# Kernel optimization log

Hardware: AMD Instinct MI355X
Metric: run time of the kernel (lower is better)

## Reference

```python
import jax, jax.numpy as jnp
import numpy as np

N, T_IN, PRE_LEN = 4096, 8, 12
E, H = 64, 128
MAX_NEI_DIS = 5.0


def _lstm_cell(x, h, c, Wih, Whh, bih, bhh):
    # torch.nn.LSTMCell math; gate order i, f, g, o
    gates = x @ Wih.T + bih + h @ Whh.T + bhh
    i, f, g, o = jnp.split(gates, 4, axis=-1)
    i = jax.nn.sigmoid(i)
    f = jax.nn.sigmoid(f)
    g = jnp.tanh(g)
    o = jax.nn.sigmoid(o)
    c_new = f * c + i * g
    return o * jnp.tanh(c_new), c_new


def _social_pool(pos, hidden):
    # sum hidden[j] over j with ||pos_j - pos_i|| < MAX_NEI_DIS (self included)
    d2 = jnp.sum((pos[:, None, :] - pos[None, :, :]) ** 2, axis=-1)  # [N,N]
    mask = (d2 < MAX_NEI_DIS * MAX_NEI_DIS).astype(hidden.dtype)
    return mask @ hidden  # [N,H]


def setup_inputs() -> dict:
    key = jax.random.key(0)
    ks = jax.random.split(key, 10)
    tracks = jax.random.normal(ks[0], (N, T_IN, 2), dtype=jnp.float32) * 20.0
    s = 0.05
    return {
        "tracks": tracks,
        "We": jax.random.normal(ks[1], (E, 2), dtype=jnp.float32) * s,
        "be": jax.random.normal(ks[2], (E,), dtype=jnp.float32) * s,
        "Wih": jax.random.normal(ks[3], (4 * H, H + E), dtype=jnp.float32) * s,
        "Whh": jax.random.normal(ks[4], (4 * H, H), dtype=jnp.float32) * s,
        "bih": jax.random.normal(ks[5], (4 * H,), dtype=jnp.float32) * s,
        "bhh": jax.random.normal(ks[6], (4 * H,), dtype=jnp.float32) * s,
        "Wd": jax.random.normal(ks[7], (2, H), dtype=jnp.float32) * s,
        "bd": jax.random.normal(ks[8], (2,), dtype=jnp.float32) * s,
    }


def reference(tracks, We, be, Wih, Whh, bih, bhh, Wd, bd):
    n = tracks.shape[0]
    emb = lambda p: p @ We.T + be

    # ---- group_encode ----
    x0 = jnp.concatenate([emb(tracks[:, 0]), jnp.zeros((n, H), tracks.dtype)], axis=1)
    h, c = _lstm_cell(x0, jnp.zeros((n, H), tracks.dtype), jnp.zeros((n, H), tracks.dtype),
                      Wih, Whh, bih, bhh)

    def enc_step(carry, pos):
        h, c = carry
        sh = _social_pool(pos, h)
        x = jnp.concatenate([emb(pos), sh], axis=1)
        h, c = _lstm_cell(x, h, c, Wih, Whh, bih, bhh)
        return (h, c), None

    # frame_idx = 0 .. input_len-2 -> positions at frames 0..6
    enc_pos = jnp.swapaxes(tracks[:, : T_IN - 1], 0, 1)  # [7, N, 2]
    (h, c), _ = jax.lax.scan(enc_step, (h, c), enc_pos)

    # ---- decode ----
    def dec_step(carry, _):
        h, c, last = carry
        sh = _social_pool(last, h)
        x = jnp.concatenate([emb(last), sh], axis=1)
        h, c = _lstm_cell(x, h, c, Wih, Whh, bih, bhh)
        delta = h @ Wd.T + bd
        last = last + delta
        return (h, c, last), last[0]

    last = tracks[:, -1]
    _, preds0 = jax.lax.scan(dec_step, (h, c, last), None, length=PRE_LEN)
    # returned group_track[0]: original 8 frames + 12 predicted positions
    return jnp.concatenate([tracks[0], preds0], axis=0)  # [20, 2]
```

## Files before the change

### kernel.cpp

```cpp
#include <hip/hip_runtime.h>
#include <hip/hip_bf16.h>

#define N_AG   4096
#define T_IN   8
#define PRELEN 12
#define EDIM   64
#define HDIM   128
#define KTOT   320
#define GDIM   512
#define KI     10
#define LOSCALE 2048.0f

typedef _Float16 f16x8 __attribute__((ext_vector_type(8)));
typedef _Float16 f16x2 __attribute__((ext_vector_type(2)));
typedef float    f32x4 __attribute__((ext_vector_type(4)));


__global__ __launch_bounds__(256) void init_kernel(
    const float* __restrict__ tracks,
    const float* __restrict__ Wih, const float* __restrict__ Whh,
    const float* __restrict__ bih, const float* __restrict__ bhh,
    float* __restrict__ hA, float* __restrict__ hB, float* __restrict__ c,
    float* __restrict__ lastA, float* __restrict__ lastB,
    _Float16* __restrict__ WfH, _Float16* __restrict__ WfL,
    float* __restrict__ bsum, float* __restrict__ posAll,
    float* __restrict__ h16Af, float* __restrict__ h16Bf,
    float* __restrict__ out)
{
    int idx = blockIdx.x * 256 + threadIdx.x;
    hA[idx] = 0.f;
    hB[idx] = 0.f;
    c[idx]  = 0.f;
    if (idx < 262208) { h16Af[idx] = 0.f; h16Bf[idx] = 0.f; }
    if (idx < KTOT * GDIM) {
        int g = idx / KTOT, k = idx - g * KTOT;
        float val = (k < 192) ? Wih[g * 192 + k] : Whh[g * 128 + (k - 192)];
        int nt = g >> 4, ki = k >> 5;
        int ln = (g & 15) | (((k >> 3) & 3) << 4);
        int e  = k & 7;
        size_t off = (size_t)((nt * KI + ki) * 64 + ln) * 8 + e;
        _Float16 hi = (_Float16)val;
        WfH[off] = hi;
        WfL[off] = (_Float16)((val - (float)hi) * LOSCALE);
    }
    if (idx < N_AG) {
        lastA[idx * 2 + 0] = tracks[idx * 16 + 14];
        lastA[idx * 2 + 1] = tracks[idx * 16 + 15];
        lastB[idx * 2 + 0] = 0.f;
        lastB[idx * 2 + 1] = 0.f;
    }
    if (idx < GDIM) bsum[idx] = bih[idx] + bhh[idx];
    if (idx < 16)  out[idx] = tracks[idx];
    if (idx < 7 * N_AG) {
        int t = idx / N_AG, a = idx & (N_AG - 1);
        posAll[idx * 2 + 0] = tracks[a * 16 + t * 2 + 0];
        posAll[idx * 2 + 1] = tracks[a * 16 + t * 2 + 1];
    }
}

__global__ __launch_bounds__(512) void social_step(
    const float* __restrict__ pp,
    const float* __restrict__ We, const float* __restrict__ be,
    const _Float16* __restrict__ WfH, const _Float16* __restrict__ WfL,
    const float* __restrict__ bsum,
    const float* __restrict__ hIn, float* __restrict__ hOut,
    const _Float16* __restrict__ h16In, _Float16* __restrict__ h16Out,
    float* __restrict__ c,
    const float* __restrict__ lastIn, float* __restrict__ lastOut,
    const float* __restrict__ Wd, const float* __restrict__ bd,
    float* __restrict__ out,
    int firstStep, int decStep)
{
    __shared__ __align__(16) char smraw[77824];
    _Float16 (*AH)[64][8] = (_Float16(*)[64][8])smraw;
    _Float16 (*AL)[64][8] = (_Float16(*)[64][8])(smraw + 10240);
    float (*shs)[HDIM]    = (float(*)[HDIM])(smraw + 20480);
    unsigned short (*sidx)[2][512] = (unsigned short(*)[2][512])(smraw + 28672);
    float (*hs)[HDIM]     = (float(*)[HDIM])(smraw + 28672);
    float* posl           = (float*)(smraw + 45056);

    int tid  = threadIdx.x;
    int lane = tid & 63;
    int wv   = tid >> 6;
    int a0   = blockIdx.x * 16;

    if (!firstStep) {
#pragma unroll
        for (int k = 0; k < 4; k++) {
            int u = tid + k * 512;
            *(f32x4*)&posl[u * 4] = *(const f32x4*)(pp + (size_t)u * 4);
        }
        __syncthreads();

        const float2* pvl = (const float2*)posl;
        int iA = a0 + 2 * wv, iB = iA + 1;
        float2 piA = pvl[iA], piB = pvl[iB];
        unsigned long long ltmask = (1ull << lane) - 1ull;
        int cntA = 0, cntB = 0;
#pragma unroll 8
        for (int cc = 0; cc < 32; cc++) {
            int j0 = cc * 128 + 2 * lane;
            float4 q = *(const float4*)&posl[(size_t)j0 * 2];
            float dxA0 = q.x - piA.x, dyA0 = q.y - piA.y;
            float dxA1 = q.z - piA.x, dyA1 = q.w - piA.y;
            float dxB0 = q.x - piB.x, dyB0 = q.y - piB.y;
            float dxB1 = q.z - piB.x, dyB1 = q.w - piB.y;
            bool pA0 = dxA0 * dxA0 + dyA0 * dyA0 < 25.0f;
            bool pA1 = dxA1 * dxA1 + dyA1 * dyA1 < 25.0f;
            bool pB0 = dxB0 * dxB0 + dyB0 * dyB0 < 25.0f;
            bool pB1 = dxB1 * dxB1 + dyB1 * dyB1 < 25.0f;
            unsigned long long mA0 = __ballot(pA0), mA1 = __ballot(pA1);
            unsigned long long mB0 = __ballot(pB0), mB1 = __ballot(pB1);
            if (pA0) { int s = cntA + __popcll(mA0 & ltmask); if (s < 512) sidx[wv][0][s] = (unsigned short)j0; }
            cntA += __popcll(mA0);
            if (pA1) { int s = cntA + __popcll(mA1 & ltmask); if (s < 512) sidx[wv][0][s] = (unsigned short)(j0 + 1); }
            cntA += __popcll(mA1);
            if (pB0) { int s = cntB + __popcll(mB0 & ltmask); if (s < 512) sidx[wv][1][s] = (unsigned short)j0; }
            cntB += __popcll(mB0);
            if (pB1) { int s = cntB + __popcll(mB1 & ltmask); if (s < 512) sidx[wv][1][s] = (unsigned short)(j0 + 1); }
            cntB += __popcll(mB1);
        }
        if (cntA > 512) cntA = 512;
        if (cntB > 512) cntB = 512;
        int cpadA = (cntA + 15) & ~15, cpadB = (cntB + 15) & ~15;
        if (cpadA > 512) cpadA = 512;
        if (cpadB > 512) cpadB = 512;
        if (lane < cpadA - cntA) sidx[wv][0][cntA + lane] = (unsigned short)N_AG;
        if (lane < cpadB - cntB) sidx[wv][1][cntB + lane] = (unsigned short)N_AG;

        int d0 = lane * 2;
#pragma unroll
        for (int rep = 0; rep < 2; rep++) {
            int cpad = rep ? cpadB : cpadA;
            float s0 = 0.f, s1 = 0.f;
            for (int t2 = 0; t2 < cpad; t2 += 16) {
                f16x2 v[16];
#pragma unroll
                for (int r = 0; r < 16; r++) {
                    int j = sidx[wv][rep][t2 + r];
                    v[r] = *(const f16x2*)(h16In + (size_t)j * HDIM + d0);
                }
#pragma unroll
                for (int r = 0; r < 16; r++) { s0 += (float)v[r][0]; s1 += (float)v[r][1]; }
            }
            shs[2 * wv + rep][d0]     = s0;
            shs[2 * wv + rep][d0 + 1] = s1;
        }
    }
    __syncthreads();

    for (int u = tid; u < 16 * (KTOT / 8); u += 512) {
        int a = u & 15, kg = u >> 4;
        int ga = a0 + a;
        int k0 = kg * 8;
        float v[8];
        if (k0 < EDIM) {
            float px = pp[ga * 2], py = pp[ga * 2 + 1];
#pragma unroll
            for (int j = 0; j < 8; j++) {
                int k = k0 + j;
                v[j] = fmaf(px, We[k * 2], fmaf(py, We[k * 2 + 1], be[k]));
            }
        } else if (k0 < EDIM + HDIM) {
#pragma unroll
            for (int j = 0; j < 8; j++)
                v[j] = firstStep ? 0.f : shs[a][k0 - EDIM + j];
        } else {
#pragma unroll
            for (int j = 0; j < 8; j++)
                v[j] = hIn[(unsigned)ga * HDIM + (k0 - EDIM - HDIM + j)];
        }
        f16x8 hi8, lo8;
#pragma unroll
        for (int j = 0; j < 8; j++) {
            _Float16 hv = (_Float16)v[j];
            hi8[j] = hv;
            lo8[j] = (_Float16)((v[j] - (float)hv) * LOSCALE);
        }
        int ki = kg >> 2, ln = a | ((kg & 3) << 4);
        *(f16x8*)&AH[ki][ln][0] = hi8;
        *(f16x8*)&AL[ki][ln][0] = lo8;
    }
    __syncthreads();

    int dcol = wv * 16 + (lane & 15);

    f32x4 acc[4], accL[4];
#pragma unroll
    for (int g = 0; g < 4; g++) {
        float bb = bsum[dcol + g * 128];
        f32x4 z; z[0] = bb; z[1] = bb; z[2] = bb; z[3] = bb;
        acc[g] = z;
        f32x4 zz; zz[0] = 0.f; zz[1] = 0.f; zz[2] = 0.f; zz[3] = 0.f;
        accL[g] = zz;
    }
#pragma unroll
    for (int ki = 0; ki < KI; ki++) {
        f16x8 ah = *(const f16x8*)&AH[ki][lane][0];
        f16x8 al = *(const f16x8*)&AL[ki][lane][0];
#pragma unroll
        for (int g = 0; g < 4; g++) {
            int nt = wv + 8 * g;
            size_t off = (size_t)((nt * KI + ki) * 64 + lane) * 8;
            f16x8 bh = *(const f16x8*)&WfH[off];
            f16x8 bl = *(const f16x8*)&WfL[off];
            acc[g]  = __builtin_amdgcn_mfma_f32_16x16x32_f16(ah, bh, acc[g],  0, 0, 0);
            accL[g] = __builtin_amdgcn_mfma_f32_16x16x32_f16(al, bh, accL[g], 0, 0, 0);
            accL[g] = __builtin_amdgcn_mfma_f32_16x16x32_f16(ah, bl, accL[g], 0, 0, 0);
        }
    }

    const float inv = 1.0f / LOSCALE;
#pragma unroll
    for (int r = 0; r < 4; r++) {
        int alc = (lane >> 4) * 4 + r;
        int ga  = a0 + alc;
        float vi = fmaf(accL[0][r], inv, acc[0][r]);
        float vf = fmaf(accL[1][r], inv, acc[1][r]);
        float vg = fmaf(accL[2][r], inv, acc[2][r]);
        float vo = fmaf(accL[3][r], inv, acc[3][r]);
        float ig = 1.f / (1.f + expf(-vi));
        float fg = 1.f / (1.f + expf(-vf));
        float gg = tanhf(vg);
        float og = 1.f / (1.f + expf(-vo));
        float cold = c[(unsigned)ga * HDIM + dcol];
        float cn = fmaf(fg, cold, ig * gg);
        float hn = og * tanhf(cn);
        c[(unsigned)ga * HDIM + dcol]      = cn;
        hOut[(unsigned)ga * HDIM + dcol]   = hn;
        h16Out[(unsigned)ga * HDIM + dcol] = (_Float16)hn;
        hs[alc][dcol] = hn;
    }

    if (decStep >= 0) {
        __syncthreads();
        int ag = tid >> 5, comp = (tid >> 4) & 1, l16 = tid & 15;
        float s = 0.f;
#pragma unroll
        for (int j = 0; j < 8; j++) {
            int d = l16 * 8 + j;
            s += hs[ag][d] * Wd[comp * HDIM + d];
        }
        s += __shfl_down(s, 8, 16);
        s += __shfl_down(s, 4, 16);
        s += __shfl_down(s, 2, 16);
        s += __shfl_down(s, 1, 16);
        if (l16 == 0) {
            int ga = a0 + ag;
            float nl = lastIn[ga * 2 + comp] + s + bd[comp];
            lastOut[ga * 2 + comp] = nl;
            if (ga == 0) out[(8 + decStep) * 2 + comp] = nl;
        }
    }
}

extern "C" void kernel_launch(void* const* d_in, const int* in_sizes, int n_in,
                              void* d_out, int out_size, void* d_ws, size_t ws_size,
                              hipStream_t stream)
{
    const float* tracks = (const float*)d_in[0];
    const float* We     = (const float*)d_in[1];
    const float* be     = (const float*)d_in[2];
    const float* Wih    = (const float*)d_in[3];
    const float* Whh    = (const float*)d_in[4];
    const float* bih    = (const float*)d_in[5];
    const float* bhh    = (const float*)d_in[6];
    const float* Wd     = (const float*)d_in[7];
    const float* bd     = (const float*)d_in[8];
    float* out = (float*)d_out;
    float* ws  = (float*)d_ws;

    float*     hA     = ws;
    float*     hB     = ws + 524288;
    float*     c      = ws + 1048576;
    float*     lastA  = ws + 1572864;
    float*     lastB  = ws + 1581056;
    float*     bsum   = ws + 1589248;
    float*     posAll = ws + 1589760;
    _Float16*  WfH    = (_Float16*)(ws + 1647104);
    _Float16*  WfL    = (_Float16*)(ws + 1729024);
    float*     h16Af  = ws + 1810944;
    float*     h16Bf  = ws + 2073152;

    float*    hbuf[2]   = { hA, hB };
    _Float16* h16buf[2] = { (_Float16*)h16Af, (_Float16*)h16Bf };
    float*    lbuf[2]   = { lastA, lastB };

    init_kernel<<<2048, 256, 0, stream>>>(tracks, Wih, Whh, bih, bhh,
                                          hA, hB, c, lastA, lastB,
                                          WfH, WfL, bsum, posAll,
                                          h16Af, h16Bf, out);

    int k = 0;
    auto step = [&](const float* pp, const float* lin, float* lout,
                    int fs, int ds) {
        social_step<<<256, 512, 0, stream>>>(
            pp, We, be, WfH, WfL, bsum,
            hbuf[(k + 1) & 1], hbuf[k & 1],
            h16buf[(k + 1) & 1], h16buf[k & 1],
            c, lin, lout, Wd, bd, out, fs, ds);
        k++;
    };

    step(posAll, nullptr, nullptr, 1, -1);

    for (int t = 0; t < T_IN - 1; t++)
        step(posAll + (size_t)t * N_AG * 2, nullptr, nullptr, 0, -1);

    for (int s = 0; s < PRELEN; s++)
        step(lbuf[s & 1], lbuf[s & 1], lbuf[(s + 1) & 1], 0, s);
}
```

Before: 509.1 us.

## Double block size: one agent per wave for pooling, split-K MFMA across halves

```diff
diff --git a/kernel.cpp b/kernel.cpp
--- a/kernel.cpp
+++ b/kernel.cpp
@@ -58,7 +58,7 @@
     }
 }
 
-__global__ __launch_bounds__(512) void social_step(
+__global__ void __launch_bounds__(1024, 1) social_step(
     const float* __restrict__ pp,
     const float* __restrict__ We, const float* __restrict__ be,
     const _Float16* __restrict__ WfH, const _Float16* __restrict__ WfL,
@@ -75,9 +75,10 @@
     _Float16 (*AH)[64][8] = (_Float16(*)[64][8])smraw;
     _Float16 (*AL)[64][8] = (_Float16(*)[64][8])(smraw + 10240);
     float (*shs)[HDIM]    = (float(*)[HDIM])(smraw + 20480);
-    unsigned short (*sidx)[2][512] = (unsigned short(*)[2][512])(smraw + 28672);
+    unsigned short (*sidx)[512] = (unsigned short(*)[512])(smraw + 28672);
     float (*hs)[HDIM]     = (float(*)[HDIM])(smraw + 28672);
     float* posl           = (float*)(smraw + 45056);
+    float* accx           = (float*)(smraw + 45056);
 
     int tid  = threadIdx.x;
     int lane = tid & 63;
@@ -86,70 +87,53 @@
 
     if (!firstStep) {
 #pragma unroll
-        for (int k = 0; k < 4; k++) {
-            int u = tid + k * 512;
+        for (int k = 0; k < 2; k++) {
+            int u = tid + k * 1024;
             *(f32x4*)&posl[u * 4] = *(const f32x4*)(pp + (size_t)u * 4);
         }
         __syncthreads();
 
         const float2* pvl = (const float2*)posl;
-        int iA = a0 + 2 * wv, iB = iA + 1;
-        float2 piA = pvl[iA], piB = pvl[iB];
+        float2 pi = pvl[a0 + wv];
         unsigned long long ltmask = (1ull << lane) - 1ull;
-        int cntA = 0, cntB = 0;
+        int cnt = 0;
 #pragma unroll 8
         for (int cc = 0; cc < 32; cc++) {
             int j0 = cc * 128 + 2 * lane;
-            float4 q = *(const float4*)&posl[(size_t)j0 * 2];
-            float dxA0 = q.x - piA.x, dyA0 = q.y - piA.y;
-            float dxA1 = q.z - piA.x, dyA1 = q.w - piA.y;
-            float dxB0 = q.x - piB.x, dyB0 = q.y - piB.y;
-            float dxB1 = q.z - piB.x, dyB1 = q.w - piB.y;
-            bool pA0 = dxA0 * dxA0 + dyA0 * dyA0 < 25.0f;
-            bool pA1 = dxA1 * dxA1 + dyA1 * dyA1 < 25.0f;
-            bool pB0 = dxB0 * dxB0 + dyB0 * dyB0 < 25.0f;
-            bool pB1 = dxB1 * dxB1 + dyB1 * dyB1 < 25.0f;
-            unsigned long long mA0 = __ballot(pA0), mA1 = __ballot(pA1);
-            unsigned long long mB0 = __ballot(pB0), mB1 = __ballot(pB1);
-            if (pA0) { int s = cntA + __popcll(mA0 & ltmask); if (s < 512) sidx[wv][0][s] = (unsigned short)j0; }
-            cntA += __popcll(mA0);
-            if (pA1) { int s = cntA + __popcll(mA1 & ltmask); if (s < 512) sidx[wv][0][s] = (unsigned short)(j0 + 1); }
-            cntA += __popcll(mA1);
-            if (pB0) { int s = cntB + __popcll(mB0 & ltmask); if (s < 512) sidx[wv][1][s] = (unsigned short)j0; }
-            cntB += __popcll(mB0);
-            if (pB1) { int s = cntB + __popcll(mB1 & ltmask); if (s < 512) sidx[wv][1][s] = (unsigned short)(j0 + 1); }
-            cntB += __popcll(mB1);
-        }
-        if (cntA > 512) cntA = 512;
-        if (cntB > 512) cntB = 512;
-        int cpadA = (cntA + 15) & ~15, cpadB = (cntB + 15) & ~15;
-        if (cpadA > 512) cpadA = 512;
-        if (cpadB > 512) cpadB = 512;
-        if (lane < cpadA - cntA) sidx[wv][0][cntA + lane] = (unsigned short)N_AG;
-        if (lane < cpadB - cntB) sidx[wv][1][cntB + lane] = (unsigned short)N_AG;
+            float4 q4 = *(const float4*)&posl[(size_t)j0 * 2];
+            float dx0 = q4.x - pi.x, dy0 = q4.y - pi.y;
+            float dx1 = q4.z - pi.x, dy1 = q4.w - pi.y;
+            bool p0 = dx0 * dx0 + dy0 * dy0 < 25.0f;
+            bool p1 = dx1 * dx1 + dy1 * dy1 < 25.0f;
+            unsigned long long m0 = __ballot(p0), m1 = __ballot(p1);
+            if (p0) { int s = cnt + __popcll(m0 & ltmask); if (s < 512) sidx[wv][s] = (unsigned short)j0; }
+            cnt += __popcll(m0);
+            if (p1) { int s = cnt + __popcll(m1 & ltmask); if (s < 512) sidx[wv][s] = (unsigned short)(j0 + 1); }
+            cnt += __popcll(m1);
+        }
+        if (cnt > 512) cnt = 512;
+        int cpad = (cnt + 15) & ~15;
+        if (cpad > 512) cpad = 512;
+        if (lane < cpad - cnt) sidx[wv][cnt + lane] = (unsigned short)N_AG;
 
         int d0 = lane * 2;
-#pragma unroll
-        for (int rep = 0; rep < 2; rep++) {
-            int cpad = rep ? cpadB : cpadA;
-            float s0 = 0.f, s1 = 0.f;
-            for (int t2 = 0; t2 < cpad; t2 += 16) {
-                f16x2 v[16];
-#pragma unroll
-                for (int r = 0; r < 16; r++) {
-                    int j = sidx[wv][rep][t2 + r];
-                    v[r] = *(const f16x2*)(h16In + (size_t)j * HDIM + d0);
-                }
-#pragma unroll
-                for (int r = 0; r < 16; r++) { s0 += (float)v[r][0]; s1 += (float)v[r][1]; }
+        float s0 = 0.f, s1 = 0.f;
+        for (int t2 = 0; t2 < cpad; t2 += 16) {
+            f16x2 v[16];
+#pragma unroll
+            for (int r = 0; r < 16; r++) {
+                int j = sidx[wv][t2 + r];
+                v[r] = *(const f16x2*)(h16In + (size_t)j * HDIM + d0);
             }
-            shs[2 * wv + rep][d0]     = s0;
-            shs[2 * wv + rep][d0 + 1] = s1;
-        }
+#pragma unroll
+            for (int r = 0; r < 16; r++) { s0 += (float)v[r][0]; s1 += (float)v[r][1]; }
+        }
+        shs[wv][d0]     = s0;
+        shs[wv][d0 + 1] = s1;
     }
     __syncthreads();
 
-    for (int u = tid; u < 16 * (KTOT / 8); u += 512) {
+    for (int u = tid; u < 16 * (KTOT / 8); u += 1024) {
         int a = u & 15, kg = u >> 4;
         int ga = a0 + a;
         int k0 = kg * 8;
@@ -183,24 +167,28 @@
     }
     __syncthreads();
 
-    int dcol = wv * 16 + (lane & 15);
+    int q    = wv & 7;
+    int half = wv >> 3;
+    int dcol = q * 16 + (lane & 15);
+    const float inv = 1.0f / LOSCALE;
 
     f32x4 acc[4], accL[4];
 #pragma unroll
     for (int g = 0; g < 4; g++) {
-        float bb = bsum[dcol + g * 128];
+        float bb = half ? 0.f : bsum[dcol + g * 128];
         f32x4 z; z[0] = bb; z[1] = bb; z[2] = bb; z[3] = bb;
         acc[g] = z;
         f32x4 zz; zz[0] = 0.f; zz[1] = 0.f; zz[2] = 0.f; zz[3] = 0.f;
         accL[g] = zz;
     }
 #pragma unroll
-    for (int ki = 0; ki < KI; ki++) {
+    for (int kk = 0; kk < 5; kk++) {
+        int ki = half * 5 + kk;
         f16x8 ah = *(const f16x8*)&AH[ki][lane][0];
         f16x8 al = *(const f16x8*)&AL[ki][lane][0];
 #pragma unroll
         for (int g = 0; g < 4; g++) {
-            int nt = wv + 8 * g;
+            int nt = q + 8 * g;
             size_t off = (size_t)((nt * KI + ki) * 64 + lane) * 8;
             f16x8 bh = *(const f16x8*)&WfH[off];
             f16x8 bl = *(const f16x8*)&WfL[off];
@@ -209,47 +197,65 @@
             accL[g] = __builtin_amdgcn_mfma_f32_16x16x32_f16(ah, bl, accL[g], 0, 0, 0);
         }
     }
-
-    const float inv = 1.0f / LOSCALE;
-#pragma unroll
-    for (int r = 0; r < 4; r++) {
-        int alc = (lane >> 4) * 4 + r;
-        int ga  = a0 + alc;
-        float vi = fmaf(accL[0][r], inv, acc[0][r]);
-        float vf = fmaf(accL[1][r], inv, acc[1][r]);
-        float vg = fmaf(accL[2][r], inv, acc[2][r]);
-        float vo = fmaf(accL[3][r], inv, acc[3][r]);
-        float ig = 1.f / (1.f + expf(-vi));
-        float fg = 1.f / (1.f + expf(-vf));
-        float gg = tanhf(vg);
-        float og = 1.f / (1.f + expf(-vo));
-        float cold = c[(unsigned)ga * HDIM + dcol];
-        float cn = fmaf(fg, cold, ig * gg);
-        float hn = og * tanhf(cn);
-        c[(unsigned)ga * HDIM + dcol]      = cn;
-        hOut[(unsigned)ga * HDIM + dcol]   = hn;
-        h16Out[(unsigned)ga * HDIM + dcol] = (_Float16)hn;
-        hs[alc][dcol] = hn;
+#pragma unroll
+    for (int g = 0; g < 4; g++) {
+#pragma unroll
+        for (int r = 0; r < 4; r++)
+            acc[g][r] = fmaf(accL[g][r], inv, acc[g][r]);
+    }
+    if (half) {
+#pragma unroll
+        for (int g = 0; g < 4; g++)
+            *(f32x4*)&accx[(size_t)((q * 4 + g) * 64 + lane) * 4] = acc[g];
+    }
+    __syncthreads();
+
+    if (!half) {
+#pragma unroll
+        for (int g = 0; g < 4; g++) {
+            f32x4 o = *(const f32x4*)&accx[(size_t)((q * 4 + g) * 64 + lane) * 4];
+#pragma unroll
+            for (int r = 0; r < 4; r++) acc[g][r] += o[r];
+        }
+#pragma unroll
+        for (int r = 0; r < 4; r++) {
+            int alc = (lane >> 4) * 4 + r;
+            int ga  = a0 + alc;
+            float vi = acc[0][r], vf = acc[1][r], vg = acc[2][r], vo = acc[3][r];
+            float ig = 1.f / (1.f + expf(-vi));
+            float fg = 1.f / (1.f + expf(-vf));
+            float gg = tanhf(vg);
+            float og = 1.f / (1.f + expf(-vo));
+            float cold = c[(unsigned)ga * HDIM + dcol];
+            float cn = fmaf(fg, cold, ig * gg);
+            float hn = og * tanhf(cn);
+            c[(unsigned)ga * HDIM + dcol]      = cn;
+            hOut[(unsigned)ga * HDIM + dcol]   = hn;
+            h16Out[(unsigned)ga * HDIM + dcol] = (_Float16)hn;
+            hs[alc][dcol] = hn;
+        }
     }
 
     if (decStep >= 0) {
         __syncthreads();
-        int ag = tid >> 5, comp = (tid >> 4) & 1, l16 = tid & 15;
-        float s = 0.f;
-#pragma unroll
-        for (int j = 0; j < 8; j++) {
-            int d = l16 * 8 + j;
-            s += hs[ag][d] * Wd[comp * HDIM + d];
-        }
-        s += __shfl_down(s, 8, 16);
-        s += __shfl_down(s, 4, 16);
-        s += __shfl_down(s, 2, 16);
-        s += __shfl_down(s, 1, 16);
-        if (l16 == 0) {
-            int ga = a0 + ag;
-            float nl = lastIn[ga * 2 + comp] + s + bd[comp];
-            lastOut[ga * 2 + comp] = nl;
-            if (ga == 0) out[(8 + decStep) * 2 + comp] = nl;
+        if (tid < 512) {
+            int ag = tid >> 5, comp = (tid >> 4) & 1, l16 = tid & 15;
+            float s = 0.f;
+#pragma unroll
+            for (int j = 0; j < 8; j++) {
+                int d = l16 * 8 + j;
+                s += hs[ag][d] * Wd[comp * HDIM + d];
+            }
+            s += __shfl_down(s, 8, 16);
+            s += __shfl_down(s, 4, 16);
+            s += __shfl_down(s, 2, 16);
+            s += __shfl_down(s, 1, 16);
+            if (l16 == 0) {
+                int ga = a0 + ag;
+                float nl = lastIn[ga * 2 + comp] + s + bd[comp];
+                lastOut[ga * 2 + comp] = nl;
+                if (ga == 0) out[(8 + decStep) * 2 + comp] = nl;
+            }
         }
     }
 }
@@ -294,7 +300,7 @@
     int k = 0;
     auto step = [&](const float* pp, const float* lin, float* lout,
                     int fs, int ds) {
-        social_step<<<256, 512, 0, stream>>>(
+        social_step<<<256, 1024, 0, stream>>>(
             pp, We, be, WfH, WfL, bsum,
             hbuf[(k + 1) & 1], hbuf[k & 1],
             h16buf[(k + 1) & 1], h16buf[k & 1],
```

New measurement: 446.1 us. 12.4% less time.
